# Kernel optimization log

Measured on AMD Instinct MI355X. Metric: run time of the kernel, lower is better.

The kernel has to match this reference:

```python
import jax, jax.numpy as jnp
import numpy as np

WINDOW = 128
LOOK_BACKWARD = 1
LOOK_FORWARD = 0
PAD_VALUE = -1


def look_around(x, backward=LOOK_BACKWARD, forward=LOOK_FORWARD, pad_value=PAD_VALUE):
    # x: [b, windows, window_size, ...]; pad along windows axis, concat along window_size axis
    pad_width = [(0, 0)] * x.ndim
    pad_width[1] = (backward, forward)
    px = jnp.pad(x, pad_width, constant_values=pad_value)
    w = x.shape[1]
    return jnp.concatenate([px[:, i:i + w] for i in range(forward + backward + 1)], axis=2)


def rotate_half(x):
    x1, x2 = jnp.split(x, 2, axis=-1)
    return jnp.concatenate([-x2, x1], axis=-1)


def setup_inputs() -> dict:
    key = jax.random.key(0)
    k1, k2, k3 = jax.random.split(key, 3)
    B, H, N, D = 4, 16, 4096, 64
    return {
        "q": jax.random.normal(k1, (B, H, N, D), dtype=jnp.float32),
        "k": jax.random.normal(k2, (B, H, N, D), dtype=jnp.float32),
        "v": jax.random.normal(k3, (B, H, N, D), dtype=jnp.float32),
    }


def reference(q, k, v):
    B, H, N, D = q.shape
    qf = q.reshape(B * H, N, D)
    kf = k.reshape(B * H, N, D)
    vf = v.reshape(B * H, N, D)

    # --- inline rotary (SinusoidalEmbeddings + apply_rotary_pos_emb) ---
    inv_freq = 1.0 / (10000.0 ** (jnp.arange(0, D, 2, dtype=jnp.float32) / D))  # [D/2]
    t = jnp.arange(N, dtype=jnp.float32)
    half = t[:, None] * inv_freq[None, :]                      # [N, D/2]
    freqs = jnp.concatenate([half, half], axis=-1)             # [N, D]
    cos, sin = jnp.cos(freqs), jnp.sin(freqs)
    qf = qf * cos + rotate_half(qf) * sin
    kf = kf * cos + rotate_half(kf) * sin

    # --- blocked local attention ---
    w = WINDOW
    windows = N // w
    scale = D ** -0.5
    bq = qf.reshape(B * H, windows, w, D)
    bk = look_around(kf.reshape(B * H, windows, w, D))         # [bh, windows, j, D]
    bv = look_around(vf.reshape(B * H, windows, w, D))

    seq = jnp.arange(N).reshape(1, windows, w)
    bq_t = seq[..., :, None]                                   # [1, windows, w, 1]
    bq_k = look_around(seq)[..., None, :]                      # [1, windows, 1, j]

    sim = jnp.einsum('bwie,bwje->bwij', bq, bk) * scale        # [bh, windows, w, j]
    mask_value = -jnp.finfo(sim.dtype).max
    sim = jnp.where(bq_t < bq_k, mask_value, sim)              # causal mask

    attn = jax.nn.softmax(sim, axis=-1)
    out = jnp.einsum('bwij,bwje->bwie', attn, bv)              # [bh, windows, w, D]
    return out.reshape(B, H, N, D)
```

## Files before the change

### kernel.cpp

```cpp
#include <hip/hip_runtime.h>
#include <hip/hip_bf16.h>

typedef __attribute__((ext_vector_type(8))) short  short8;
typedef __attribute__((ext_vector_type(4))) short  short4v;
typedef __attribute__((ext_vector_type(4))) float  float4v;

#define MFMA_QK(A,B,C) __builtin_amdgcn_mfma_f32_16x16x32_bf16(A,B,C,0,0,0)
#define MFMA_PV(A,B,C) __builtin_amdgcn_mfma_f32_16x16x16bf16_1k(A,B,C,0,0,0)

static __device__ __forceinline__ short f2bf(float x) {
  unsigned u = __float_as_uint(x);
  u += 0x7fffu + ((u >> 16) & 1u);
  return (short)(u >> 16);
}

static __device__ __forceinline__ void rope_sc(float rev, float& sn, float& cs) {
  float fr = rev - floorf(rev);
  sn = __builtin_amdgcn_sinf(fr);
  cs = __builtin_amdgcn_cosf(fr);
}

static __device__ __forceinline__ float invfreq_rev(int idx) {
  return exp2f(-0.41524101186092034f * (float)idx) * 0.15915494309189535f;
}

#define N_ 4096
#define D_ 64
#define W_ 128

__global__ __launch_bounds__(256, 2)
void la_fused(const float* __restrict__ qg, const float* __restrict__ kg,
              const float* __restrict__ vg, float* __restrict__ outg)
{
  __shared__ __attribute__((aligned(16))) short Kl[256][72];
  __shared__ __attribute__((aligned(16))) short Vl[64][264];

  const int blk  = blockIdx.x;
  const int w    = blk & 31;
  const int bh   = blk >> 5;
  const int base = bh * (N_ * D_);
  const int tid  = threadIdx.x;

  {
    const float* kb = kg + base;
    const float* vb = vg + base;
#pragma unroll
    for (int it = 0; it < 8; ++it) {
      int tau = it * 256 + tid;
      int j   = tau >> 3;
      int d0  = (tau & 7) << 2;
      int g   = w * W_ - W_ + j;
      float klo[4], khi[4], vlo[4], vhi[4];
      if (g < 0) {
#pragma unroll
        for (int dd = 0; dd < 4; ++dd) { klo[dd]=khi[dd]=vlo[dd]=vhi[dd] = -1.0f; }
      } else {
        float4v a   = *(const float4v*)(kb + g * D_ + d0);
        float4v b   = *(const float4v*)(kb + g * D_ + d0 + 32);
        float4v va  = *(const float4v*)(vb + g * D_ + d0);
        float4v vb2 = *(const float4v*)(vb + g * D_ + d0 + 32);
        const float t = (float)g;
#pragma unroll
        for (int dd = 0; dd < 4; ++dd) {
          float sn, cs; rope_sc(t * invfreq_rev(d0 + dd), sn, cs);
          klo[dd] = a[dd] * cs - b[dd] * sn;
          khi[dd] = b[dd] * cs + a[dd] * sn;
          vlo[dd] = va[dd]; vhi[dd] = vb2[dd];
        }
      }
      short4v k0 = { f2bf(klo[0]), f2bf(klo[1]), f2bf(klo[2]), f2bf(klo[3]) };
      short4v k1 = { f2bf(khi[0]), f2bf(khi[1]), f2bf(khi[2]), f2bf(khi[3]) };
      *(short4v*)&Kl[j][d0]      = k0;
      *(short4v*)&Kl[j][d0 + 32] = k1;
#pragma unroll
      for (int dd = 0; dd < 4; ++dd) {
        Vl[d0 + dd][j]      = f2bf(vlo[dd]);
        Vl[d0 + 32 + dd][j] = f2bf(vhi[dd]);
      }
    }
  }
  __syncthreads();

  const int lane = tid & 63;
  const int wv   = tid >> 6;
  const int il   = lane & 15;
  const int qd   = lane >> 4;

  short8 qf[2][2];
#pragma unroll
  for (int ii = 0; ii < 2; ++ii) {
    const int rw = wv * 32 + ii * 16 + il;
    const int n  = w * W_ + rw;
    const float* qr = qg + base + n * D_ + qd * 8;
    float4v x0 = *(const float4v*)(qr);
    float4v x1 = *(const float4v*)(qr + 4);
    float4v y0 = *(const float4v*)(qr + 32);
    float4v y1 = *(const float4v*)(qr + 36);
    float lo[8], hi[8];
    const float t = (float)n;
#pragma unroll
    for (int jj = 0; jj < 8; ++jj) {
      const int d = qd * 8 + jj;
      float xx = (jj < 4) ? x0[jj & 3] : x1[jj & 3];
      float yy = (jj < 4) ? y0[jj & 3] : y1[jj & 3];
      float sn, cs; rope_sc(t * invfreq_rev(d), sn, cs);
      lo[jj] = xx * cs - yy * sn;
      hi[jj] = yy * cs + xx * sn;
    }
    qf[ii][0] = short8{ f2bf(lo[0]),f2bf(lo[1]),f2bf(lo[2]),f2bf(lo[3]),
                        f2bf(lo[4]),f2bf(lo[5]),f2bf(lo[6]),f2bf(lo[7]) };
    qf[ii][1] = short8{ f2bf(hi[0]),f2bf(hi[1]),f2bf(hi[2]),f2bf(hi[3]),
                        f2bf(hi[4]),f2bf(hi[5]),f2bf(hi[6]),f2bf(hi[7]) };
  }

  float4v S[2][16];
#pragma unroll
  for (int ii = 0; ii < 2; ++ii)
#pragma unroll
    for (int t = 0; t < 16; ++t) { float4v z = {0.f,0.f,0.f,0.f}; S[ii][t] = z; }

#pragma unroll
  for (int t = 0; t < 16; ++t) {
    short8 a0 = *(const short8*)&Kl[t * 16 + il][qd * 8];
    short8 a1 = *(const short8*)&Kl[t * 16 + il][32 + qd * 8];
#pragma unroll
    for (int ii = 0; ii < 2; ++ii) {
      S[ii][t] = MFMA_QK(a0, qf[ii][0], S[ii][t]);
      S[ii][t] = MFMA_QK(a1, qf[ii][1], S[ii][t]);
    }
  }

  short4v P[2][16];
  float   invsum[2];
#pragma unroll
  for (int ii = 0; ii < 2; ++ii) {
    const int rw = wv * 32 + ii * 16 + il;
    float mx = -3.0e38f;
#pragma unroll
    for (int t = 0; t < 16; ++t) {
#pragma unroll
      for (int r = 0; r < 4; ++r) {
        const int j = t * 16 + qd * 4 + r;
        float s = S[ii][t][r] * 0.125f;
        if (j > rw + 128) s = -3.0e38f;
        S[ii][t][r] = s;
        mx = fmaxf(mx, s);
      }
    }
    mx = fmaxf(mx, __shfl_xor(mx, 16));
    mx = fmaxf(mx, __shfl_xor(mx, 32));
    float sum = 0.0f;
#pragma unroll
    for (int t = 0; t < 16; ++t) {
#pragma unroll
      for (int r = 0; r < 4; ++r) {
        float p = __expf(S[ii][t][r] - mx);
        S[ii][t][r] = p;
        sum += p;
      }
    }
    sum += __shfl_xor(sum, 16);
    sum += __shfl_xor(sum, 32);
    invsum[ii] = 1.0f / sum;
#pragma unroll
    for (int t = 0; t < 16; ++t) {
      P[ii][t] = short4v{ f2bf(S[ii][t][0]), f2bf(S[ii][t][1]),
                          f2bf(S[ii][t][2]), f2bf(S[ii][t][3]) };
    }
  }

  float4v O[2][4];
#pragma unroll
  for (int ii = 0; ii < 2; ++ii)
#pragma unroll
    for (int dt = 0; dt < 4; ++dt) { float4v z = {0.f,0.f,0.f,0.f}; O[ii][dt] = z; }

#pragma unroll
  for (int c = 0; c < 16; ++c) {
    short4v af[4];
#pragma unroll
    for (int dt = 0; dt < 4; ++dt)
      af[dt] = *(const short4v*)&Vl[dt * 16 + il][c * 16 + qd * 4];
#pragma unroll
    for (int dt = 0; dt < 4; ++dt) {
      O[0][dt] = MFMA_PV(af[dt], P[0][c], O[0][dt]);
      O[1][dt] = MFMA_PV(af[dt], P[1][c], O[1][dt]);
    }
  }

#pragma unroll
  for (int ii = 0; ii < 2; ++ii) {
    const int n = w * W_ + wv * 32 + ii * 16 + il;
    float* op = outg + base + n * D_;
    const float inv = invsum[ii];
#pragma unroll
    for (int dt = 0; dt < 4; ++dt) {
      float4v o = O[ii][dt];
      o[0] *= inv; o[1] *= inv; o[2] *= inv; o[3] *= inv;
      *(float4v*)(op + dt * 16 + qd * 4) = o;
    }
  }
}

extern "C" void kernel_launch(void* const* d_in, const int* in_sizes, int n_in,
                              void* d_out, int out_size, void* d_ws, size_t ws_size,
                              hipStream_t stream)
{
  const float* q = (const float*)d_in[0];
  const float* k = (const float*)d_in[1];
  const float* v = (const float*)d_in[2];
  float* out = (float*)d_out;
  la_fused<<<dim3(64 * 32), dim3(256), 0, stream>>>(q, k, v, out);
}
```

Baseline: 227.8 us.

## Split key window into two tiles with online softmax and causal tile skipping

Keys and values are staged and processed in two 128-row tiles, previous window then current window, with a running max and sum (online softmax) instead of one 256-row tile. Causally masked 16-column tiles in the diagonal block are skipped per wave, which cuts MFMA and exp work. Halving shared memory and the register footprint allows raising launch bounds to 4 blocks per CU, and the V tile in LDS gets an XOR swizzle to reduce bank conflicts. The costs are an extra barrier between tiles, rescaling of the accumulators, and wave imbalance on the diagonal tile.

```diff
diff --git a/kernel.cpp b/kernel.cpp
--- a/kernel.cpp
+++ b/kernel.cpp
@@ -1,5 +1,4 @@
 #include <hip/hip_runtime.h>
-#include <hip/hip_bf16.h>
 
 typedef __attribute__((ext_vector_type(8))) short  short8;
 typedef __attribute__((ext_vector_type(4))) short  short4v;
@@ -28,59 +27,18 @@
 #define D_ 64
 #define W_ 128
 
-__global__ __launch_bounds__(256, 2)
+__global__ __launch_bounds__(256, 4)
 void la_fused(const float* __restrict__ qg, const float* __restrict__ kg,
               const float* __restrict__ vg, float* __restrict__ outg)
 {
-  __shared__ __attribute__((aligned(16))) short Kl[256][72];
-  __shared__ __attribute__((aligned(16))) short Vl[64][264];
+  __shared__ __attribute__((aligned(16))) short Kl[128][72];
+  __shared__ __attribute__((aligned(16))) short Vl[64][132];
 
   const int blk  = blockIdx.x;
   const int w    = blk & 31;
   const int bh   = blk >> 5;
   const int base = bh * (N_ * D_);
   const int tid  = threadIdx.x;
-
-  {
-    const float* kb = kg + base;
-    const float* vb = vg + base;
-#pragma unroll
-    for (int it = 0; it < 8; ++it) {
-      int tau = it * 256 + tid;
-      int j   = tau >> 3;
-      int d0  = (tau & 7) << 2;
-      int g   = w * W_ - W_ + j;
-      float klo[4], khi[4], vlo[4], vhi[4];
-      if (g < 0) {
-#pragma unroll
-        for (int dd = 0; dd < 4; ++dd) { klo[dd]=khi[dd]=vlo[dd]=vhi[dd] = -1.0f; }
-      } else {
-        float4v a   = *(const float4v*)(kb + g * D_ + d0);
-        float4v b   = *(const float4v*)(kb + g * D_ + d0 + 32);
-        float4v va  = *(const float4v*)(vb + g * D_ + d0);
-        float4v vb2 = *(const float4v*)(vb + g * D_ + d0 + 32);
-        const float t = (float)g;
-#pragma unroll
-        for (int dd = 0; dd < 4; ++dd) {
-          float sn, cs; rope_sc(t * invfreq_rev(d0 + dd), sn, cs);
-          klo[dd] = a[dd] * cs - b[dd] * sn;
-          khi[dd] = b[dd] * cs + a[dd] * sn;
-          vlo[dd] = va[dd]; vhi[dd] = vb2[dd];
-        }
-      }
-      short4v k0 = { f2bf(klo[0]), f2bf(klo[1]), f2bf(klo[2]), f2bf(klo[3]) };
-      short4v k1 = { f2bf(khi[0]), f2bf(khi[1]), f2bf(khi[2]), f2bf(khi[3]) };
-      *(short4v*)&Kl[j][d0]      = k0;
-      *(short4v*)&Kl[j][d0 + 32] = k1;
-#pragma unroll
-      for (int dd = 0; dd < 4; ++dd) {
-        Vl[d0 + dd][j]      = f2bf(vlo[dd]);
-        Vl[d0 + 32 + dd][j] = f2bf(vhi[dd]);
-      }
-    }
-  }
-  __syncthreads();
-
   const int lane = tid & 63;
   const int wv   = tid >> 6;
   const int il   = lane & 15;
@@ -113,78 +71,137 @@
                         f2bf(hi[4]),f2bf(hi[5]),f2bf(hi[6]),f2bf(hi[7]) };
   }
 
-  float4v S[2][16];
-#pragma unroll
-  for (int ii = 0; ii < 2; ++ii)
-#pragma unroll
-    for (int t = 0; t < 16; ++t) { float4v z = {0.f,0.f,0.f,0.f}; S[ii][t] = z; }
-
-#pragma unroll
-  for (int t = 0; t < 16; ++t) {
-    short8 a0 = *(const short8*)&Kl[t * 16 + il][qd * 8];
-    short8 a1 = *(const short8*)&Kl[t * 16 + il][32 + qd * 8];
+  float4v O[2][4];
+  float   m_run[2] = { -3.0e38f, -3.0e38f };
+  float   s_run[2] = { 0.f, 0.f };
+  short4v P[2][8];
+
+  const float* kb = kg + base;
+  const float* vb = vg + base;
+
+#pragma unroll
+  for (int kt = 0; kt < 2; ++kt) {
+    if (kt) __syncthreads();
+
+#pragma unroll
+    for (int it = 0; it < 4; ++it) {
+      const int tau = it * 256 + tid;
+      const int j   = tau >> 3;
+      const int d0  = (tau & 7) << 2;
+      const int g   = (w - 1 + kt) * W_ + j;
+      float klo[4], khi[4], vlo[4], vhi[4];
+      if (g < 0) {
+#pragma unroll
+        for (int dd = 0; dd < 4; ++dd) { klo[dd]=khi[dd]=vlo[dd]=vhi[dd] = -1.0f; }
+      } else {
+        float4v a   = *(const float4v*)(kb + g * D_ + d0);
+        float4v b   = *(const float4v*)(kb + g * D_ + d0 + 32);
+        float4v va  = *(const float4v*)(vb + g * D_ + d0);
+        float4v vb2 = *(const float4v*)(vb + g * D_ + d0 + 32);
+        const float t = (float)g;
+#pragma unroll
+        for (int dd = 0; dd < 4; ++dd) {
+          float sn, cs; rope_sc(t * invfreq_rev(d0 + dd), sn, cs);
+          klo[dd] = a[dd] * cs - b[dd] * sn;
+          khi[dd] = b[dd] * cs + a[dd] * sn;
+          vlo[dd] = va[dd]; vhi[dd] = vb2[dd];
+        }
+      }
+      short4v k0 = { f2bf(klo[0]), f2bf(klo[1]), f2bf(klo[2]), f2bf(klo[3]) };
+      short4v k1 = { f2bf(khi[0]), f2bf(khi[1]), f2bf(khi[2]), f2bf(khi[3]) };
+      *(short4v*)&Kl[j][d0]      = k0;
+      *(short4v*)&Kl[j][d0 + 32] = k1;
+      const int j4  = j >> 2;
+      const int jlo = j & 3;
+#pragma unroll
+      for (int dd = 0; dd < 4; ++dd) {
+        const int r0 = d0 + dd, r1 = r0 + 32;
+        Vl[r0][((j4 ^ (r0 >> 4)) << 2) | jlo] = f2bf(vlo[dd]);
+        Vl[r1][((j4 ^ (r1 >> 4)) << 2) | jlo] = f2bf(vhi[dd]);
+      }
+    }
+    __syncthreads();
+
+    const int tpv = kt ? (2 * wv + 2) : 8;
+    float corr[2];
+
 #pragma unroll
     for (int ii = 0; ii < 2; ++ii) {
-      S[ii][t] = MFMA_QK(a0, qf[ii][0], S[ii][t]);
-      S[ii][t] = MFMA_QK(a1, qf[ii][1], S[ii][t]);
-    }
-  }
-
-  short4v P[2][16];
-  float   invsum[2];
-#pragma unroll
-  for (int ii = 0; ii < 2; ++ii) {
-    const int rw = wv * 32 + ii * 16 + il;
-    float mx = -3.0e38f;
-#pragma unroll
-    for (int t = 0; t < 16; ++t) {
-#pragma unroll
-      for (int r = 0; r < 4; ++r) {
-        const int j = t * 16 + qd * 4 + r;
-        float s = S[ii][t][r] * 0.125f;
-        if (j > rw + 128) s = -3.0e38f;
-        S[ii][t][r] = s;
-        mx = fmaxf(mx, s);
-      }
-    }
-    mx = fmaxf(mx, __shfl_xor(mx, 16));
-    mx = fmaxf(mx, __shfl_xor(mx, 32));
-    float sum = 0.0f;
-#pragma unroll
-    for (int t = 0; t < 16; ++t) {
-#pragma unroll
-      for (int r = 0; r < 4; ++r) {
-        float p = __expf(S[ii][t][r] - mx);
-        S[ii][t][r] = p;
-        sum += p;
-      }
-    }
-    sum += __shfl_xor(sum, 16);
-    sum += __shfl_xor(sum, 32);
-    invsum[ii] = 1.0f / sum;
-#pragma unroll
-    for (int t = 0; t < 16; ++t) {
-      P[ii][t] = short4v{ f2bf(S[ii][t][0]), f2bf(S[ii][t][1]),
-                          f2bf(S[ii][t][2]), f2bf(S[ii][t][3]) };
-    }
-  }
-
-  float4v O[2][4];
-#pragma unroll
-  for (int ii = 0; ii < 2; ++ii)
-#pragma unroll
-    for (int dt = 0; dt < 4; ++dt) { float4v z = {0.f,0.f,0.f,0.f}; O[ii][dt] = z; }
-
-#pragma unroll
-  for (int c = 0; c < 16; ++c) {
-    short4v af[4];
-#pragma unroll
-    for (int dt = 0; dt < 4; ++dt)
-      af[dt] = *(const short4v*)&Vl[dt * 16 + il][c * 16 + qd * 4];
-#pragma unroll
-    for (int dt = 0; dt < 4; ++dt) {
-      O[0][dt] = MFMA_PV(af[dt], P[0][c], O[0][dt]);
-      O[1][dt] = MFMA_PV(af[dt], P[1][c], O[1][dt]);
+      const int rw = wv * 32 + ii * 16 + il;
+      const int tq = kt ? (2 * wv + 1 + ii) : 8;
+      float4v S[8];
+#pragma unroll
+      for (int t = 0; t < 8; ++t) if (t < tq) { float4v z = {0.f,0.f,0.f,0.f}; S[t] = z; }
+#pragma unroll
+      for (int t = 0; t < 8; ++t) if (t < tq) {
+        const short8 a0 = *(const short8*)&Kl[t * 16 + il][qd * 8];
+        const short8 a1 = *(const short8*)&Kl[t * 16 + il][32 + qd * 8];
+        S[t] = MFMA_QK(a0, qf[ii][0], S[t]);
+        S[t] = MFMA_QK(a1, qf[ii][1], S[t]);
+      }
+      float mx = -3.0e38f;
+#pragma unroll
+      for (int t = 0; t < 8; ++t) if (t < tq) {
+#pragma unroll
+        for (int r = 0; r < 4; ++r) {
+          float s = S[t][r] * 0.125f;
+          if (kt && (t * 16 + qd * 4 + r) > rw) s = -3.0e38f;
+          S[t][r] = s;
+          mx = fmaxf(mx, s);
+        }
+      }
+      mx = fmaxf(mx, __shfl_xor(mx, 16));
+      mx = fmaxf(mx, __shfl_xor(mx, 32));
+      const float mnew = fmaxf(m_run[ii], mx);
+      corr[ii] = __expf(m_run[ii] - mnew);
+      m_run[ii] = mnew;
+      float sum = 0.f;
+#pragma unroll
+      for (int t = 0; t < 8; ++t) {
+        if (t < tq) {
+          float p0 = __expf(S[t][0] - mnew);
+          float p1 = __expf(S[t][1] - mnew);
+          float p2 = __expf(S[t][2] - mnew);
+          float p3 = __expf(S[t][3] - mnew);
+          sum += (p0 + p1) + (p2 + p3);
+          P[ii][t] = short4v{ f2bf(p0), f2bf(p1), f2bf(p2), f2bf(p3) };
+        } else if (t < tpv) {
+          P[ii][t] = short4v{ 0, 0, 0, 0 };
+        }
+      }
+      sum += __shfl_xor(sum, 16);
+      sum += __shfl_xor(sum, 32);
+      s_run[ii] = s_run[ii] * corr[ii] + sum;
+    }
+
+    if (kt == 0) {
+#pragma unroll
+      for (int ii = 0; ii < 2; ++ii)
+#pragma unroll
+        for (int dt = 0; dt < 4; ++dt) { float4v z = {0.f,0.f,0.f,0.f}; O[ii][dt] = z; }
+    } else {
+#pragma unroll
+      for (int ii = 0; ii < 2; ++ii) {
+        const float c0 = corr[ii];
+#pragma unroll
+        for (int dt = 0; dt < 4; ++dt) {
+          O[ii][dt][0] *= c0; O[ii][dt][1] *= c0;
+          O[ii][dt][2] *= c0; O[ii][dt][3] *= c0;
+        }
+      }
+    }
+
+#pragma unroll
+    for (int c = 0; c < 8; ++c) if (c < tpv) {
+      short4v af[4];
+#pragma unroll
+      for (int dt = 0; dt < 4; ++dt)
+        af[dt] = *(const short4v*)&Vl[dt * 16 + il][((c * 4 + qd) ^ dt) << 2];
+#pragma unroll
+      for (int dt = 0; dt < 4; ++dt) {
+        O[0][dt] = MFMA_PV(af[dt], P[0][c], O[0][dt]);
+        O[1][dt] = MFMA_PV(af[dt], P[1][c], O[1][dt]);
+      }
     }
   }
 
@@ -192,7 +209,7 @@
   for (int ii = 0; ii < 2; ++ii) {
     const int n = w * W_ + wv * 32 + ii * 16 + il;
     float* op = outg + base + n * D_;
-    const float inv = invsum[ii];
+    const float inv = 1.0f / s_run[ii];
 #pragma unroll
     for (int dt = 0; dt < 4; ++dt) {
       float4v o = O[ii][dt];
```

New measurement: 322.4 us. 1.41x slower.
